# Kernel tuning notes

Hardware: AMD Instinct MI355X
Metric: run time of the kernel (lower is better)

## Reference

```python
import jax, jax.numpy as jnp
import numpy as np
from itertools import product

B, D, H, W = 2, 32, 256, 256
N = 150000
C_IN, C_MID, C_OUT = 16, 32, 64
STRIDE, PAD, K = 2, 1, 3
DO = (D + 2 * PAD - K) // STRIDE + 1
HO = (H + 2 * PAD - K) // STRIDE + 1
WO = (W + 2 * PAD - K) // STRIDE + 1
EPS = 1e-5


def setup_inputs() -> dict:
    key = jax.random.key(0)
    ks = jax.random.split(key, 8)
    # unique active voxel coords via permutation of linear grid indices
    lin = jax.random.permutation(ks[0], B * D * H * W)[:N]
    b = lin // (D * H * W); r = lin % (D * H * W)
    z = r // (H * W); r = r % (H * W)
    y = r // W; x = r % W
    coords = jnp.stack([b, z, y, x], axis=1).astype(jnp.int32)  # [N,4] = (batch,z,y,x)
    feats = jax.random.normal(ks[1], (N, C_IN), jnp.float32)
    W1 = jax.random.normal(ks[2], (27, C_IN, C_MID), jnp.float32) * 0.08
    W2 = jax.random.normal(ks[3], (27, C_MID, C_MID), jnp.float32) * 0.06
    W3 = jax.random.normal(ks[4], (27, C_MID, C_OUT), jnp.float32) * 0.06
    b1 = jnp.zeros((C_MID,), jnp.float32); g1 = jnp.ones((C_MID,), jnp.float32); be1 = jnp.zeros((C_MID,), jnp.float32)
    b2 = jnp.zeros((C_MID,), jnp.float32); g2 = jnp.ones((C_MID,), jnp.float32); be2 = jnp.zeros((C_MID,), jnp.float32)
    b3 = jnp.zeros((C_OUT,), jnp.float32); g3 = jnp.ones((C_OUT,), jnp.float32); be3 = jnp.zeros((C_OUT,), jnp.float32)
    return dict(feats=feats, coords=coords, W1=W1, b1=b1, g1=g1, be1=be1,
                W2=W2, b2=b2, g2=g2, be2=be2, W3=W3, b3=b3, g3=g3, be3=be3)


def _bn_relu(x, g, b):
    # BatchNorm1d (training batch stats, biased var) over active voxels + ReLU
    m = x.mean(0)
    v = ((x - m) ** 2).mean(0)
    return jax.nn.relu((x - m) * jax.lax.rsqrt(v + EPS) * g + b)


def _subm_conv(feats, coords, grid, Wk, bias):
    # submanifold conv: gather neighbor features per kernel offset, GEMM, accumulate
    bb, zz, yy, xx = coords[:, 0], coords[:, 1], coords[:, 2], coords[:, 3]
    acc = jnp.zeros((feats.shape[0], Wk.shape[-1]), feats.dtype)
    for ki, (dz, dy, dx) in enumerate(product((-1, 0, 1), repeat=3)):
        nz, ny, nx = zz + dz, yy + dy, xx + dx
        valid = (nz >= 0) & (nz < D) & (ny >= 0) & (ny < H) & (nx >= 0) & (nx < W)
        lin = ((bb * D + jnp.clip(nz, 0, D - 1)) * H + jnp.clip(ny, 0, H - 1)) * W + jnp.clip(nx, 0, W - 1)
        nidx = jnp.where(valid, grid[lin], -1)
        gathered = jnp.where((nidx >= 0)[:, None], feats[jnp.maximum(nidx, 0)], 0.0)
        acc = acc + gathered @ Wk[ki]
    return acc + bias


def _sparse_down_conv(feats, coords, Wk, bias):
    # stride-2 SparseConv3d as GEMM + scatter-add into downsampled dense grid; mask = active outputs
    bb, zz, yy, xx = coords[:, 0], coords[:, 1], coords[:, 2], coords[:, 3]
    M = B * DO * HO * WO
    out = jnp.zeros((M, Wk.shape[-1]), feats.dtype)
    cnt = jnp.zeros((M,), jnp.int32)
    for ki, (kz, ky, kx) in enumerate(product(range(K), repeat=3)):
        oz, oy, ox = zz + PAD - kz, yy + PAD - ky, xx + PAD - kx
        valid = ((oz % STRIDE == 0) & (oy % STRIDE == 0) & (ox % STRIDE == 0) &
                 (oz >= 0) & (oy >= 0) & (ox >= 0) &
                 (oz // STRIDE < DO) & (oy // STRIDE < HO) & (ox // STRIDE < WO))
        lin = ((bb * DO + jnp.clip(oz // STRIDE, 0, DO - 1)) * HO
               + jnp.clip(oy // STRIDE, 0, HO - 1)) * WO + jnp.clip(ox // STRIDE, 0, WO - 1)
        lin = jnp.where(valid, lin, 0)
        contrib = jnp.where(valid[:, None], feats @ Wk[ki], 0.0)
        out = out.at[lin].add(contrib)
        cnt = cnt.at[lin].add(valid.astype(jnp.int32))
    mask = cnt > 0
    out = jnp.where(mask[:, None], out + bias, 0.0)
    return out, mask


def reference(feats, coords, W1, b1, g1, be1, W2, b2, g2, be2, W3, b3, g3, be3):
    lin0 = ((coords[:, 0] * D + coords[:, 1]) * H + coords[:, 2]) * W + coords[:, 3]
    grid = jnp.full((B * D * H * W,), -1, jnp.int32).at[lin0].set(jnp.arange(N, dtype=jnp.int32))
    x = _bn_relu(_subm_conv(feats, coords, grid, W1, b1), g1, be1)
    x = _bn_relu(_subm_conv(x, coords, grid, W2, b2), g2, be2)
    out, mask = _sparse_down_conv(x, coords, W3, b3)
    nact = jnp.maximum(mask.sum(), 1).astype(out.dtype)
    m = out.sum(0) / nact  # inactive rows are zero
    v = jnp.where(mask[:, None], (out - m) ** 2, 0.0).sum(0) / nact
    out = jax.nn.relu((out - m) * jax.lax.rsqrt(v + EPS) * g3 + be3)
    out = jnp.where(mask[:, None], out, 0.0)
    return out.reshape(B, DO, HO, WO, C_OUT)
```

## Files before the change

kernel.cpp:

```cpp
#include <hip/hip_runtime.h>

#define B_   2
#define D_   32
#define H_   256
#define W_   256
#define N_   150000
#define CIN  16
#define CMID 32
#define COUT 64
#define DO_  16
#define HO_  128
#define WO_  128
#define M_   (B_*DO_*HO_*WO_)
#define EPSf 1e-5f
#define NB_DOWN 8192
#define NREP 64

typedef _Float16 h2 __attribute__((ext_vector_type(2)));
__device__ inline h2 as_h2(unsigned u) { union { unsigned u; h2 h; } x; x.u = u; return x.h; }

#if defined(__has_builtin) && __has_builtin(__builtin_amdgcn_fdot2)
__device__ inline float dot2(unsigned f, unsigned w, float acc) {
    return __builtin_amdgcn_fdot2(as_h2(f), as_h2(w), acc, false);
}
#else
__device__ inline float dot2(unsigned f, unsigned w, float acc) {
    const h2 a = as_h2(f), b = as_h2(w);
    return fmaf((float)a.x, (float)b.x, fmaf((float)a.y, (float)b.y, acc));
}
#endif

__device__ inline unsigned hpk(float a, float b) {
    union { _Float16 h[2]; unsigned u; } x;
    x.h[0] = (_Float16)a; x.h[1] = (_Float16)b; return x.u;
}

__global__ __launch_bounds__(256) void k_scatter(const int* __restrict__ coords,
                                                 int* __restrict__ grid) {
    int i = blockIdx.x * 256 + threadIdx.x;
    if (i >= N_) return;
    const int4 c = *(const int4*)(coords + 4 * (size_t)i);
    grid[((c.x * D_ + c.y) * H_ + c.z) * W_ + c.w] = i;
}

__global__ __launch_bounds__(256) void k_twisth(const float* __restrict__ W1,
                                                const float* __restrict__ W2,
                                                const float* __restrict__ W3,
                                                uint4* __restrict__ Wh1,
                                                uint4* __restrict__ Wh2,
                                                uint4* __restrict__ Wh3) {
    const int t = blockIdx.x * 256 + threadIdx.x;
    if (t < 1728) {
        const int ki = t / 64, r = t % 64, half = r >> 5, sub = r & 31;
        const float* base = W1 + ki * 512 + (half * 8) * 32 + sub;
        uint4 o;
        o.x = hpk(base[0],   base[32]);
        o.y = hpk(base[64],  base[96]);
        o.z = hpk(base[128], base[160]);
        o.w = hpk(base[192], base[224]);
        Wh1[(ki * 2 + half) * 32 + sub] = o;
    } else if (t < 1728 + 3456) {
        const int u = t - 1728;
        const int ki = u / 128, r = u % 128, qh = r >> 5, sub = r & 31;
        const int half = qh >> 1, q = qh & 1;
        const float* base = W2 + ki * 1024 + (half * 16 + q * 8) * 32 + sub;
        uint4 o;
        o.x = hpk(base[0],   base[32]);
        o.y = hpk(base[64],  base[96]);
        o.z = hpk(base[128], base[160]);
        o.w = hpk(base[192], base[224]);
        Wh2[((ki * 2 + half) * 2 + q) * 32 + sub] = o;
    } else if (t < 1728 + 3456 + 6912) {
        const int u = t - 5184;
        const int ki = u / 256, r = u % 256, q = r >> 6, lane = r & 63;
        const float* base = W3 + ki * 2048 + (q * 8) * 64 + lane;
        uint4 o;
        o.x = hpk(base[0],   base[64]);
        o.y = hpk(base[128], base[192]);
        o.z = hpk(base[256], base[320]);
        o.w = hpk(base[384], base[448]);
        Wh3[(ki * 4 + q) * 64 + lane] = o;
    }
}

__global__ __launch_bounds__(256) void k_feat16(const float* __restrict__ F,
                                                unsigned* __restrict__ F16) {
    const int i = blockIdx.x * 256 + threadIdx.x;
    if (i >= N_ * CIN / 4) return;
    const float4 v = ((const float4*)F)[i];
    uint2 o; o.x = hpk(v.x, v.y); o.y = hpk(v.z, v.w);
    ((uint2*)F16)[i] = o;
}

template <int CI>
__global__ __launch_bounds__(256) void k_subm(const unsigned* __restrict__ X16,
                                              const int* __restrict__ coords,
                                              const int* __restrict__ grid,
                                              const uint4* __restrict__ Wh,
                                              const float* __restrict__ bias,
                                              float* __restrict__ Y) {
    constexpr int NQ = CI / 16;
    const int pid  = (blockIdx.x * 256 + threadIdx.x) >> 6;
    const int lane = threadIdx.x & 63;
    const int sub  = lane & 31;
    const int half = lane >> 5;
    const int iA   = pid * 2;

    const int4 cA = *(const int4*)(coords + 4 * (size_t)iA);
    const int4 cB = *(const int4*)(coords + 4 * (size_t)(iA + 1));
    const int4 cc = half ? cB : cA;

    int nidx = -1;
    if (sub < 27) {
        const int nz = cc.y + sub / 9 - 1;
        const int ny = cc.z + (sub / 3) % 3 - 1;
        const int nx = cc.w + sub % 3 - 1;
        if ((unsigned)nz < (unsigned)D_ && (unsigned)ny < (unsigned)H_ &&
            (unsigned)nx < (unsigned)W_)
            nidx = grid[((cc.x * D_ + nz) * H_ + ny) * W_ + nx];
    }
    const unsigned long long act = __ballot(nidx >= 0);
    unsigned int actA = (unsigned int)(act & 0x7FFFFFFull);
    unsigned int actB = (unsigned int)((act >> 32) & 0x7FFFFFFull);

    float accA = 0.f, accB = 0.f;

    while (actA | actB) {
        if (actA) {
            const int ki = __builtin_ctz(actA); actA &= actA - 1;
            const int ni = __shfl(nidx, ki, 64);
            const uint4* __restrict__ f =
                (const uint4*)(X16 + (size_t)ni * (CI / 2) + half * (CI / 4));
            const uint4* __restrict__ wb = Wh + ((size_t)(ki * 2 + half)) * NQ * 32 + sub;
#pragma unroll
            for (int q = 0; q < NQ; ++q) {
                const uint4 fu = f[q];
                const uint4 wu = wb[q * 32];
                accA = dot2(fu.x, wu.x, accA);
                accA = dot2(fu.y, wu.y, accA);
                accA = dot2(fu.z, wu.z, accA);
                accA = dot2(fu.w, wu.w, accA);
            }
        }
        if (actB) {
            const int ki = __builtin_ctz(actB); actB &= actB - 1;
            const int ni = __shfl(nidx, ki + 32, 64);
            const uint4* __restrict__ f =
                (const uint4*)(X16 + (size_t)ni * (CI / 2) + half * (CI / 4));
            const uint4* __restrict__ wb = Wh + ((size_t)(ki * 2 + half)) * NQ * 32 + sub;
#pragma unroll
            for (int q = 0; q < NQ; ++q) {
                const uint4 fu = f[q];
                const uint4 wu = wb[q * 32];
                accB = dot2(fu.x, wu.x, accB);
                accB = dot2(fu.y, wu.y, accB);
                accB = dot2(fu.z, wu.z, accB);
                accB = dot2(fu.w, wu.w, accB);
            }
        }
    }

    accA += __shfl_xor(accA, 32, 64);
    accB += __shfl_xor(accB, 32, 64);
    const float outv = (half ? accB : accA) + bias[sub];
    Y[(size_t)(iA + half) * 32 + sub] = outv;
}

__global__ __launch_bounds__(256) void k_down(const unsigned* __restrict__ X16,
                                              const int* __restrict__ grid,
                                              const uint4* __restrict__ Wh3,
                                              const float* __restrict__ bias,
                                              _Float16* __restrict__ Yh,
                                              unsigned char* __restrict__ mask,
                                              float* __restrict__ slab0,
                                              int* __restrict__ nacts) {
    const int b    = blockIdx.x;
    const int swz  = (b & 7) * (NB_DOWN / 8) + (b >> 3);
    const int tid  = threadIdx.x;
    const int wv   = tid >> 6;
    const int lane = tid & 63;
    const int sub  = lane & 31;
    const int half = lane >> 5;

    const int vox0 = swz * 64;
    const int ox0  = vox0 & 127;
    int t = vox0 >> 7;
    const int oy = t & 127; t >>= 7;
    const int oz = t & 15;
    const int bb = t >> 4;

    __shared__ int   gl[9][132];
    __shared__ float sd[256];
    __shared__ int   scnt[4];

    const int gx0 = 2 * ox0 - 1;
    for (int e = tid; e < 9 * 132; e += 256) {
        const int r  = e / 132, xo = e % 132;
        const int z  = 2 * oz - 1 + r / 3;
        const int y  = 2 * oy - 1 + r % 3;
        const int x  = gx0 + xo;
        int v = -1;
        if ((unsigned)z < (unsigned)D_ && (unsigned)y < (unsigned)H_ &&
            (unsigned)x < (unsigned)W_ && xo < 129)
            v = grid[((bb * D_ + z) * H_ + y) * W_ + x];
        gl[r][xo] = v;
    }
    __syncthreads();

    const int dz = sub / 9, dy = (sub / 3) % 3, dx = sub % 3;
    const int row = (sub < 27) ? dz * 3 + dy : 0;

    const float bv = bias[lane];
    float s = 0.f, s2 = 0.f;
    int cnt = 0;

    for (int it = 0; it < 8; ++it) {
        const int pr = wv * 8 + it;
        const int xo = 2 * (pr * 2 + half) + dx;
        const int nidx = (sub < 27) ? gl[row][xo] : -1;

        const unsigned long long act = __ballot(nidx >= 0);
        unsigned int actA = (unsigned int)(act & 0x7FFFFFFull);
        unsigned int actB = (unsigned int)((act >> 32) & 0x7FFFFFFull);
        const int mkA = actA ? 1 : 0;
        const int mkB = actB ? 1 : 0;

        float accA = 0.f, accB = 0.f;
        while (actA | actB) {
            if (actA) {
                const int ki = __builtin_ctz(actA); actA &= actA - 1;
                const int ni = __builtin_amdgcn_readfirstlane(__shfl(nidx, ki, 64));
                const uint4* __restrict__ fS = (const uint4*)(X16 + (size_t)ni * 16);
                const uint4* __restrict__ wb = Wh3 + (size_t)ki * 256 + lane;
#pragma unroll
                for (int q = 0; q < 4; ++q) {
                    const uint4 fu = fS[q];
                    const uint4 wu = wb[q * 64];
                    accA = dot2(fu.x, wu.x, accA);
                    accA = dot2(fu.y, wu.y, accA);
                    accA = dot2(fu.z, wu.z, accA);
                    accA = dot2(fu.w, wu.w, accA);
                }
            }
            if (actB) {
                const int ki = __builtin_ctz(actB); actB &= actB - 1;
                const int ni = __builtin_amdgcn_readfirstlane(__shfl(nidx, ki + 32, 64));
                const uint4* __restrict__ fS = (const uint4*)(X16 + (size_t)ni * 16);
                const uint4* __restrict__ wb = Wh3 + (size_t)ki * 256 + lane;
#pragma unroll
                for (int q = 0; q < 4; ++q) {
                    const uint4 fu = fS[q];
                    const uint4 wu = wb[q * 64];
                    accB = dot2(fu.x, wu.x, accB);
                    accB = dot2(fu.y, wu.y, accB);
                    accB = dot2(fu.z, wu.z, accB);
                    accB = dot2(fu.w, wu.w, accB);
                }
            }
        }

        const int vA = vox0 + pr * 2;
        const float oA = mkA ? accA + bv : 0.f;
        const float oB = mkB ? accB + bv : 0.f;
        Yh[(size_t)vA * COUT + lane]       = (_Float16)oA;
        Yh[(size_t)(vA + 1) * COUT + lane] = (_Float16)oB;
        if (lane == 0) {
            mask[vA]     = (unsigned char)mkA;
            mask[vA + 1] = (unsigned char)mkB;
            cnt += mkA + mkB;
        }
        s  += oA + oB;
        s2 += oA * oA + oB * oB;
    }

    float* __restrict__ slab = slab0 + (size_t)(b & (NREP - 1)) * 128;
    sd[tid] = s;
    if (lane == 0) scnt[wv] = cnt;
    __syncthreads();
    if (tid < 64) atomicAdd(slab + tid, sd[tid] + sd[tid + 64] + sd[tid + 128] + sd[tid + 192]);
    __syncthreads();
    sd[tid] = s2;
    __syncthreads();
    if (tid < 64) atomicAdd(slab + 64 + tid, sd[tid] + sd[tid + 64] + sd[tid + 128] + sd[tid + 192]);
    if (tid == 0) atomicAdd(nacts + (b & (NREP - 1)), scnt[0] + scnt[1] + scnt[2] + scnt[3]);
}

template <int C>
__global__ __launch_bounds__(256) void k_stats(const float* __restrict__ Y,
                                               long n_elems,
                                               float* __restrict__ slab0) {
    __shared__ float sdata[256];
    const int t = threadIdx.x;
    const long stride = (long)gridDim.x * 256;
    float s = 0.f, s2 = 0.f;
    for (long idx = (long)blockIdx.x * 256 + t; idx < n_elems; idx += stride) {
        const float v = Y[idx];
        s += v; s2 += v * v;
    }
    float* __restrict__ slab = slab0 + (size_t)(blockIdx.x & (NREP - 1)) * 2 * C;
    sdata[t] = s; __syncthreads();
    for (int off = 128; off >= C; off >>= 1) {
        if (t < off) sdata[t] += sdata[t + off];
        __syncthreads();
    }
    if (t < C) atomicAdd(slab + t, sdata[t]);
    __syncthreads();
    sdata[t] = s2; __syncthreads();
    for (int off = 128; off >= C; off >>= 1) {
        if (t < off) sdata[t] += sdata[t + off];
        __syncthreads();
    }
    if (t < C) atomicAdd(slab + C + t, sdata[t]);
}

template <int C>
__global__ void k_finslab(const float* __restrict__ slab0,
                          const float* __restrict__ g,
                          const float* __restrict__ be,
                          float n, float* __restrict__ ss) {
    const int c = threadIdx.x;
    if (c >= C) return;
    float sm = 0.f, s2 = 0.f;
    for (int r = 0; r < NREP; ++r) {
        sm += slab0[r * 2 * C + c];
        s2 += slab0[r * 2 * C + C + c];
    }
    const float m  = sm / n;
    const float v  = s2 / n - m * m;
    const float sc = g[c] * rsqrtf(v + EPSf);
    ss[c]     = sc;
    ss[C + c] = be[c] - m * sc;
}

__global__ void k_finstats3(const float* __restrict__ slab0,
                            const int* __restrict__ nacts,
                            const float* __restrict__ g,
                            const float* __restrict__ be,
                            float* __restrict__ ss) {
    const int c = threadIdx.x;
    if (c >= 64) return;
    float sm = 0.f, s2 = 0.f;
    int na = 0;
    for (int r = 0; r < NREP; ++r) {
        sm += slab0[r * 128 + c];
        s2 += slab0[r * 128 + 64 + c];
        na += nacts[r];
    }
    const float n  = (float)(na > 0 ? na : 1);
    const float m  = sm / n;
    const float v  = s2 / n - m * m;
    const float sc = g[c] * rsqrtf(v + EPSf);
    ss[c]      = sc;
    ss[64 + c] = be[c] - m * sc;
}

template <int C>
__global__ __launch_bounds__(256) void k_norm16(const float* __restrict__ Y,
                                                const float* __restrict__ ss,
                                                unsigned* __restrict__ Xo16, long n4) {
    const long t = (long)blockIdx.x * 256 + threadIdx.x;
    if (t >= n4) return;
    const float4 y = ((const float4*)Y)[t];
    const int ch = (int)((t * 4) % C);
    float ox = fmaxf(fmaf(y.x, ss[ch],     ss[C + ch]),     0.f);
    float oy = fmaxf(fmaf(y.y, ss[ch + 1], ss[C + ch + 1]), 0.f);
    float oz = fmaxf(fmaf(y.z, ss[ch + 2], ss[C + ch + 2]), 0.f);
    float ow = fmaxf(fmaf(y.w, ss[ch + 3], ss[C + ch + 3]), 0.f);
    uint2 o; o.x = hpk(ox, oy); o.y = hpk(oz, ow);
    ((uint2*)Xo16)[t] = o;
}

__global__ __launch_bounds__(256) void k_norm3(const _Float16* __restrict__ Yh,
                                               const unsigned char* __restrict__ mask,
                                               const float* __restrict__ ss,
                                               float* __restrict__ out) {
    const long n4 = (long)M_ * COUT / 4;
    const long t = (long)blockIdx.x * 256 + threadIdx.x;
    if (t >= n4) return;
    const long vox = t >> 4;
    const int ch = (int)((t * 4) & 63);
    float4 o;
    if (mask[vox]) {
        const uint2 yu = *(const uint2*)(Yh + t * 4);
        const h2 ylo = as_h2(yu.x), yhi = as_h2(yu.y);
        o.x = fmaxf(fmaf((float)ylo.x, ss[ch],     ss[64 + ch]),     0.f);
        o.y = fmaxf(fmaf((float)ylo.y, ss[ch + 1], ss[64 + ch + 1]), 0.f);
        o.z = fmaxf(fmaf((float)yhi.x, ss[ch + 2], ss[64 + ch + 2]), 0.f);
        o.w = fmaxf(fmaf((float)yhi.y, ss[ch + 3], ss[64 + ch + 3]), 0.f);
    } else {
        o.x = o.y = o.z = o.w = 0.f;
    }
    ((float4*)out)[t] = o;
}

extern "C" void kernel_launch(void* const* d_in, const int* in_sizes, int n_in,
                              void* d_out, int out_size, void* d_ws, size_t ws_size,
                              hipStream_t stream) {
    const float* feats = (const float*)d_in[0];
    const int*   coords = (const int*)d_in[1];
    const float* W1 = (const float*)d_in[2];
    const float* b1 = (const float*)d_in[3];
    const float* g1 = (const float*)d_in[4];
    const float* be1 = (const float*)d_in[5];
    const float* W2 = (const float*)d_in[6];
    const float* b2 = (const float*)d_in[7];
    const float* g2 = (const float*)d_in[8];
    const float* be2 = (const float*)d_in[9];
    const float* W3 = (const float*)d_in[10];
    const float* b3 = (const float*)d_in[11];
    const float* g3 = (const float*)d_in[12];
    const float* be3 = (const float*)d_in[13];
    float* out = (float*)d_out;

    char* ws = (char*)d_ws;
    const size_t gridBytes = (size_t)B_ * D_ * H_ * W_ * 4;
    const size_t bufBytes  = (size_t)N_ * CMID * 4;
    const size_t bufHBytes = (size_t)N_ * CMID * 2;
    const size_t YhBytes   = (size_t)M_ * COUT * 2;
    int*       grid   = (int*)ws;
    float*     bufA   = (float*)(ws + gridBytes);
    unsigned*  bufH   = (unsigned*)(ws + gridBytes + bufBytes);
    unsigned*  feat16 = (unsigned*)(ws + gridBytes + bufBytes + bufHBytes);
    _Float16*  Yh     = (_Float16*)(ws + gridBytes + bufBytes + bufHBytes +
                                    (size_t)N_ * CIN * 2);
    unsigned char* mask = (unsigned char*)(ws + gridBytes + bufBytes + bufHBytes +
                                           (size_t)N_ * CIN * 2 + YhBytes);
    float* stats = (float*)(ws + gridBytes + bufBytes + bufHBytes +
                            (size_t)N_ * CIN * 2 + YhBytes + (size_t)M_);

    float* ss1   = stats;
    float* ss2   = stats + 64;
    float* ss3   = stats + 128;
    float* slab1 = stats + 1024;
    float* slab2 = stats + 1024 + NREP * 64;
    float* slab3 = stats + 1024 + NREP * 128;
    int*   nacts = (int*)(stats + 1024 + NREP * 256);
    uint4* Wh1 = (uint4*)(stats + 32768);
    uint4* Wh2 = Wh1 + 1728;
    uint4* Wh3 = Wh2 + 3456;

    hipMemsetAsync(grid, 0xFF, gridBytes, stream);
    hipMemsetAsync(stats + 1024, 0, (NREP * 256 + NREP) * 4, stream);

    k_scatter<<<(N_ + 255) / 256, 256, 0, stream>>>(coords, grid);
    k_twisth<<<(12096 + 255) / 256, 256, 0, stream>>>(W1, W2, W3, Wh1, Wh2, Wh3);
    k_feat16<<<(N_ * CIN / 4 + 255) / 256, 256, 0, stream>>>(feats, feat16);

    const int nb_subm = 75000 / 4;
    k_subm<CIN><<<nb_subm, 256, 0, stream>>>(feat16, coords, grid, Wh1, b1, bufA);
    k_stats<CMID><<<512, 256, 0, stream>>>(bufA, (long)N_ * CMID, slab1);
    k_finslab<CMID><<<1, 64, 0, stream>>>(slab1, g1, be1, (float)N_, ss1);
    k_norm16<CMID><<<(N_ * CMID / 4 + 255) / 256, 256, 0, stream>>>(bufA, ss1, bufH,
                                                                    (long)N_ * CMID / 4);

    k_subm<CMID><<<nb_subm, 256, 0, stream>>>(bufH, coords, grid, Wh2, b2, bufA);
    k_stats<CMID><<<512, 256, 0, stream>>>(bufA, (long)N_ * CMID, slab2);
    k_finslab<CMID><<<1, 64, 0, stream>>>(slab2, g2, be2, (float)N_, ss2);
    k_norm16<CMID><<<(N_ * CMID / 4 + 255) / 256, 256, 0, stream>>>(bufA, ss2, bufH,
                                                                    (long)N_ * CMID / 4);

    k_down<<<NB_DOWN, 256, 0, stream>>>(bufH, grid, Wh3, b3, Yh, mask, slab3, nacts);
    k_finstats3<<<1, 64, 0, stream>>>(slab3, nacts, g3, be3, ss3);
    k_norm3<<<(M_ * COUT / 4) / 256, 256, 0, stream>>>(Yh, mask, ss3, out);
}
```

Baseline: 265.0 us.

## Fuse BN stats into submanifold conv, store fp16 pre-norm, process four voxels per wave

Each subm conv block now reduces per-channel sum and sum-of-squares in shared memory and atomically adds them into the stats slab, which removes the separate k_stats pass over the fp32 output. The intermediate output is stored as fp16 instead of fp32, halving the write and re-read traffic for k_norm16. Both subm and down-conv kernels now handle four voxels per wave instead of two, interleaving more independent gather chains to hide latency. In exchange there is fp16 rounding before the batch-norm stats and apply, plus more atomics and block syncs.

```diff
diff --git a/kernel.cpp b/kernel.cpp
--- a/kernel.cpp
+++ b/kernel.cpp
@@ -98,72 +98,103 @@
                                               const int* __restrict__ grid,
                                               const uint4* __restrict__ Wh,
                                               const float* __restrict__ bias,
-                                              float* __restrict__ Y) {
+                                              _Float16* __restrict__ Yp,
+                                              float* __restrict__ slab0) {
     constexpr int NQ = CI / 16;
-    const int pid  = (blockIdx.x * 256 + threadIdx.x) >> 6;
+    const int wid  = (blockIdx.x * 256 + threadIdx.x) >> 6;
     const int lane = threadIdx.x & 63;
     const int sub  = lane & 31;
     const int half = lane >> 5;
-    const int iA   = pid * 2;
-
-    const int4 cA = *(const int4*)(coords + 4 * (size_t)iA);
-    const int4 cB = *(const int4*)(coords + 4 * (size_t)(iA + 1));
-    const int4 cc = half ? cB : cA;
-
-    int nidx = -1;
-    if (sub < 27) {
-        const int nz = cc.y + sub / 9 - 1;
-        const int ny = cc.z + (sub / 3) % 3 - 1;
-        const int nx = cc.w + sub % 3 - 1;
-        if ((unsigned)nz < (unsigned)D_ && (unsigned)ny < (unsigned)H_ &&
-            (unsigned)nx < (unsigned)W_)
-            nidx = grid[((cc.x * D_ + nz) * H_ + ny) * W_ + nx];
-    }
-    const unsigned long long act = __ballot(nidx >= 0);
-    unsigned int actA = (unsigned int)(act & 0x7FFFFFFull);
-    unsigned int actB = (unsigned int)((act >> 32) & 0x7FFFFFFull);
-
-    float accA = 0.f, accB = 0.f;
-
-    while (actA | actB) {
-        if (actA) {
-            const int ki = __builtin_ctz(actA); actA &= actA - 1;
-            const int ni = __shfl(nidx, ki, 64);
-            const uint4* __restrict__ f =
-                (const uint4*)(X16 + (size_t)ni * (CI / 2) + half * (CI / 4));
-            const uint4* __restrict__ wb = Wh + ((size_t)(ki * 2 + half)) * NQ * 32 + sub;
+    const int i0   = wid * 4;
+
+    int nidx01 = -1, nidx23 = -1;
+    {
+        const int4 cc = *(const int4*)(coords + 4 * (size_t)(i0 + half));
+        if (sub < 27) {
+            const int nz = cc.y + sub / 9 - 1;
+            const int ny = cc.z + (sub / 3) % 3 - 1;
+            const int nx = cc.w + sub % 3 - 1;
+            if ((unsigned)nz < (unsigned)D_ && (unsigned)ny < (unsigned)H_ &&
+                (unsigned)nx < (unsigned)W_)
+                nidx01 = grid[((cc.x * D_ + nz) * H_ + ny) * W_ + nx];
+        }
+    }
+    {
+        const int4 cc = *(const int4*)(coords + 4 * (size_t)(i0 + 2 + half));
+        if (sub < 27) {
+            const int nz = cc.y + sub / 9 - 1;
+            const int ny = cc.z + (sub / 3) % 3 - 1;
+            const int nx = cc.w + sub % 3 - 1;
+            if ((unsigned)nz < (unsigned)D_ && (unsigned)ny < (unsigned)H_ &&
+                (unsigned)nx < (unsigned)W_)
+                nidx23 = grid[((cc.x * D_ + nz) * H_ + ny) * W_ + nx];
+        }
+    }
+    const unsigned long long a01 = __ballot(nidx01 >= 0);
+    const unsigned long long a23 = __ballot(nidx23 >= 0);
+    unsigned m0 = (unsigned)a01 & 0x7FFFFFFu;
+    unsigned m1 = (unsigned)(a01 >> 32) & 0x7FFFFFFu;
+    unsigned m2 = (unsigned)a23 & 0x7FFFFFFu;
+    unsigned m3 = (unsigned)(a23 >> 32) & 0x7FFFFFFu;
+
+    float acc0 = 0.f, acc1 = 0.f, acc2 = 0.f, acc3 = 0.f;
+
+    auto tap = [&](int ki, int ni, float& acc) {
+        const uint4* __restrict__ f =
+            (const uint4*)(X16 + (size_t)ni * (CI / 2) + half * (CI / 4));
+        const uint4* __restrict__ wb = Wh + ((size_t)(ki * 2 + half)) * NQ * 32 + sub;
 #pragma unroll
-            for (int q = 0; q < NQ; ++q) {
-                const uint4 fu = f[q];
-                const uint4 wu = wb[q * 32];
-                accA = dot2(fu.x, wu.x, accA);
-                accA = dot2(fu.y, wu.y, accA);
-                accA = dot2(fu.z, wu.z, accA);
-                accA = dot2(fu.w, wu.w, accA);
-            }
-        }
-        if (actB) {
-            const int ki = __builtin_ctz(actB); actB &= actB - 1;
-            const int ni = __shfl(nidx, ki + 32, 64);
-            const uint4* __restrict__ f =
-                (const uint4*)(X16 + (size_t)ni * (CI / 2) + half * (CI / 4));
-            const uint4* __restrict__ wb = Wh + ((size_t)(ki * 2 + half)) * NQ * 32 + sub;
+        for (int q = 0; q < NQ; ++q) {
+            const uint4 fu = f[q];
+            const uint4 wu = wb[q * 32];
+            acc = dot2(fu.x, wu.x, acc);
+            acc = dot2(fu.y, wu.y, acc);
+            acc = dot2(fu.z, wu.z, acc);
+            acc = dot2(fu.w, wu.w, acc);
+        }
+    };
+
+    while (m0 | m1 | m2 | m3) {
+        if (m0) { const int ki = __builtin_ctz(m0); m0 &= m0 - 1;
+                  tap(ki, __shfl(nidx01, ki, 64),      acc0); }
+        if (m1) { const int ki = __builtin_ctz(m1); m1 &= m1 - 1;
+                  tap(ki, __shfl(nidx01, ki + 32, 64), acc1); }
+        if (m2) { const int ki = __builtin_ctz(m2); m2 &= m2 - 1;
+                  tap(ki, __shfl(nidx23, ki, 64),      acc2); }
+        if (m3) { const int ki = __builtin_ctz(m3); m3 &= m3 - 1;
+                  tap(ki, __shfl(nidx23, ki + 32, 64), acc3); }
+    }
+
+    acc0 += __shfl_xor(acc0, 32, 64);
+    acc1 += __shfl_xor(acc1, 32, 64);
+    acc2 += __shfl_xor(acc2, 32, 64);
+    acc3 += __shfl_xor(acc3, 32, 64);
+    const float bv  = bias[sub];
+    const float o01 = (half ? acc1 : acc0) + bv;
+    const float o23 = (half ? acc3 : acc2) + bv;
+    Yp[(size_t)(i0 + half) * 32 + sub]     = (_Float16)o01;
+    Yp[(size_t)(i0 + 2 + half) * 32 + sub] = (_Float16)o23;
+
+    __shared__ float sd[256];
+    const int tid = threadIdx.x;
+    float* __restrict__ slab = slab0 + (size_t)(blockIdx.x & (NREP - 1)) * 64;
+    sd[tid] = o01 + o23;
+    __syncthreads();
+    if (tid < 32) {
+        float t = 0.f;
 #pragma unroll
-            for (int q = 0; q < NQ; ++q) {
-                const uint4 fu = f[q];
-                const uint4 wu = wb[q * 32];
-                accB = dot2(fu.x, wu.x, accB);
-                accB = dot2(fu.y, wu.y, accB);
-                accB = dot2(fu.z, wu.z, accB);
-                accB = dot2(fu.w, wu.w, accB);
-            }
-        }
-    }
-
-    accA += __shfl_xor(accA, 32, 64);
-    accB += __shfl_xor(accB, 32, 64);
-    const float outv = (half ? accB : accA) + bias[sub];
-    Y[(size_t)(iA + half) * 32 + sub] = outv;
+        for (int k = 0; k < 8; ++k) t += sd[tid + 32 * k];
+        atomicAdd(slab + tid, t);
+    }
+    __syncthreads();
+    sd[tid] = o01 * o01 + o23 * o23;
+    __syncthreads();
+    if (tid < 32) {
+        float t = 0.f;
+#pragma unroll
+        for (int k = 0; k < 8; ++k) t += sd[tid + 32 * k];
+        atomicAdd(slab + 32 + tid, t);
+    }
 }
 
 __global__ __launch_bounds__(256) void k_down(const unsigned* __restrict__ X16,
@@ -214,63 +245,63 @@
     float s = 0.f, s2 = 0.f;
     int cnt = 0;
 
-    for (int it = 0; it < 8; ++it) {
-        const int pr = wv * 8 + it;
-        const int xo = 2 * (pr * 2 + half) + dx;
-        const int nidx = (sub < 27) ? gl[row][xo] : -1;
-
-        const unsigned long long act = __ballot(nidx >= 0);
-        unsigned int actA = (unsigned int)(act & 0x7FFFFFFull);
-        unsigned int actB = (unsigned int)((act >> 32) & 0x7FFFFFFull);
-        const int mkA = actA ? 1 : 0;
-        const int mkB = actB ? 1 : 0;
-
-        float accA = 0.f, accB = 0.f;
-        while (actA | actB) {
-            if (actA) {
-                const int ki = __builtin_ctz(actA); actA &= actA - 1;
-                const int ni = __builtin_amdgcn_readfirstlane(__shfl(nidx, ki, 64));
-                const uint4* __restrict__ fS = (const uint4*)(X16 + (size_t)ni * 16);
-                const uint4* __restrict__ wb = Wh3 + (size_t)ki * 256 + lane;
+    auto tap = [&](int ki, int ni, float& acc) {
+        const uint4* __restrict__ fS = (const uint4*)(X16 + (size_t)ni * 16);
+        const uint4* __restrict__ wb = Wh3 + (size_t)ki * 256 + lane;
 #pragma unroll
-                for (int q = 0; q < 4; ++q) {
-                    const uint4 fu = fS[q];
-                    const uint4 wu = wb[q * 64];
-                    accA = dot2(fu.x, wu.x, accA);
-                    accA = dot2(fu.y, wu.y, accA);
-                    accA = dot2(fu.z, wu.z, accA);
-                    accA = dot2(fu.w, wu.w, accA);
-                }
-            }
-            if (actB) {
-                const int ki = __builtin_ctz(actB); actB &= actB - 1;
-                const int ni = __builtin_amdgcn_readfirstlane(__shfl(nidx, ki + 32, 64));
-                const uint4* __restrict__ fS = (const uint4*)(X16 + (size_t)ni * 16);
-                const uint4* __restrict__ wb = Wh3 + (size_t)ki * 256 + lane;
-#pragma unroll
-                for (int q = 0; q < 4; ++q) {
-                    const uint4 fu = fS[q];
-                    const uint4 wu = wb[q * 64];
-                    accB = dot2(fu.x, wu.x, accB);
-                    accB = dot2(fu.y, wu.y, accB);
-                    accB = dot2(fu.z, wu.z, accB);
-                    accB = dot2(fu.w, wu.w, accB);
-                }
-            }
-        }
-
-        const int vA = vox0 + pr * 2;
-        const float oA = mkA ? accA + bv : 0.f;
-        const float oB = mkB ? accB + bv : 0.f;
-        Yh[(size_t)vA * COUT + lane]       = (_Float16)oA;
-        Yh[(size_t)(vA + 1) * COUT + lane] = (_Float16)oB;
+        for (int q = 0; q < 4; ++q) {
+            const uint4 fu = fS[q];
+            const uint4 wu = wb[q * 64];
+            acc = dot2(fu.x, wu.x, acc);
+            acc = dot2(fu.y, wu.y, acc);
+            acc = dot2(fu.z, wu.z, acc);
+            acc = dot2(fu.w, wu.w, acc);
+        }
+    };
+
+    for (int it = 0; it < 4; ++it) {
+        const int v0 = wv * 16 + it * 4;
+        const int n01 = (sub < 27) ? gl[row][2 * (v0 + half) + dx] : -1;
+        const int n23 = (sub < 27) ? gl[row][2 * (v0 + 2 + half) + dx] : -1;
+        const unsigned long long a01 = __ballot(n01 >= 0);
+        const unsigned long long a23 = __ballot(n23 >= 0);
+        unsigned m0 = (unsigned)a01 & 0x7FFFFFFu;
+        unsigned m1 = (unsigned)(a01 >> 32) & 0x7FFFFFFu;
+        unsigned m2 = (unsigned)a23 & 0x7FFFFFFu;
+        unsigned m3 = (unsigned)(a23 >> 32) & 0x7FFFFFFu;
+        const int mk0 = m0 ? 1 : 0, mk1 = m1 ? 1 : 0;
+        const int mk2 = m2 ? 1 : 0, mk3 = m3 ? 1 : 0;
+
+        float ac0 = 0.f, ac1 = 0.f, ac2 = 0.f, ac3 = 0.f;
+        while (m0 | m1 | m2 | m3) {
+            if (m0) { const int ki = __builtin_ctz(m0); m0 &= m0 - 1;
+                      tap(ki, __builtin_amdgcn_readfirstlane(__shfl(n01, ki, 64)),      ac0); }
+            if (m1) { const int ki = __builtin_ctz(m1); m1 &= m1 - 1;
+                      tap(ki, __builtin_amdgcn_readfirstlane(__shfl(n01, ki + 32, 64)), ac1); }
+            if (m2) { const int ki = __builtin_ctz(m2); m2 &= m2 - 1;
+                      tap(ki, __builtin_amdgcn_readfirstlane(__shfl(n23, ki, 64)),      ac2); }
+            if (m3) { const int ki = __builtin_ctz(m3); m3 &= m3 - 1;
+                      tap(ki, __builtin_amdgcn_readfirstlane(__shfl(n23, ki + 32, 64)), ac3); }
+        }
+
+        const int vg = vox0 + v0;
+        const float o0 = mk0 ? ac0 + bv : 0.f;
+        const float o1 = mk1 ? ac1 + bv : 0.f;
+        const float o2 = mk2 ? ac2 + bv : 0.f;
+        const float o3 = mk3 ? ac3 + bv : 0.f;
+        Yh[(size_t)vg * COUT + lane]       = (_Float16)o0;
+        Yh[(size_t)(vg + 1) * COUT + lane] = (_Float16)o1;
+        Yh[(size_t)(vg + 2) * COUT + lane] = (_Float16)o2;
+        Yh[(size_t)(vg + 3) * COUT + lane] = (_Float16)o3;
         if (lane == 0) {
-            mask[vA]     = (unsigned char)mkA;
-            mask[vA + 1] = (unsigned char)mkB;
-            cnt += mkA + mkB;
-        }
-        s  += oA + oB;
-        s2 += oA * oA + oB * oB;
+            mask[vg]     = (unsigned char)mk0;
+            mask[vg + 1] = (unsigned char)mk1;
+            mask[vg + 2] = (unsigned char)mk2;
+            mask[vg + 3] = (unsigned char)mk3;
+            cnt += mk0 + mk1 + mk2 + mk3;
+        }
+        s  += o0 + o1 + o2 + o3;
+        s2 += o0 * o0 + o1 * o1 + o2 * o2 + o3 * o3;
     }
 
     float* __restrict__ slab = slab0 + (size_t)(b & (NREP - 1)) * 128;
@@ -283,34 +314,6 @@
     __syncthreads();
     if (tid < 64) atomicAdd(slab + 64 + tid, sd[tid] + sd[tid + 64] + sd[tid + 128] + sd[tid + 192]);
     if (tid == 0) atomicAdd(nacts + (b & (NREP - 1)), scnt[0] + scnt[1] + scnt[2] + scnt[3]);
-}
-
-template <int C>
-__global__ __launch_bounds__(256) void k_stats(const float* __restrict__ Y,
-                                               long n_elems,
-                                               float* __restrict__ slab0) {
-    __shared__ float sdata[256];
-    const int t = threadIdx.x;
-    const long stride = (long)gridDim.x * 256;
-    float s = 0.f, s2 = 0.f;
-    for (long idx = (long)blockIdx.x * 256 + t; idx < n_elems; idx += stride) {
-        const float v = Y[idx];
-        s += v; s2 += v * v;
-    }
-    float* __restrict__ slab = slab0 + (size_t)(blockIdx.x & (NREP - 1)) * 2 * C;
-    sdata[t] = s; __syncthreads();
-    for (int off = 128; off >= C; off >>= 1) {
-        if (t < off) sdata[t] += sdata[t + off];
-        __syncthreads();
-    }
-    if (t < C) atomicAdd(slab + t, sdata[t]);
-    __syncthreads();
-    sdata[t] = s2; __syncthreads();
-    for (int off = 128; off >= C; off >>= 1) {
-        if (t < off) sdata[t] += sdata[t + off];
-        __syncthreads();
-    }
-    if (t < C) atomicAdd(slab + C + t, sdata[t]);
 }
 
 template <int C>
@@ -355,17 +358,18 @@
 }
 
 template <int C>
-__global__ __launch_bounds__(256) void k_norm16(const float* __restrict__ Y,
+__global__ __launch_bounds__(256) void k_norm16(const unsigned* __restrict__ Yp2,
                                                 const float* __restrict__ ss,
                                                 unsigned* __restrict__ Xo16, long n4) {
     const long t = (long)blockIdx.x * 256 + threadIdx.x;
     if (t >= n4) return;
-    const float4 y = ((const float4*)Y)[t];
+    const uint2 y = ((const uint2*)Yp2)[t];
+    const h2 lo = as_h2(y.x), hi = as_h2(y.y);
     const int ch = (int)((t * 4) % C);
-    float ox = fmaxf(fmaf(y.x, ss[ch],     ss[C + ch]),     0.f);
-    float oy = fmaxf(fmaf(y.y, ss[ch + 1], ss[C + ch + 1]), 0.f);
-    float oz = fmaxf(fmaf(y.z, ss[ch + 2], ss[C + ch + 2]), 0.f);
-    float ow = fmaxf(fmaf(y.w, ss[ch + 3], ss[C + ch + 3]), 0.f);
+    float ox = fmaxf(fmaf((float)lo.x, ss[ch],     ss[C + ch]),     0.f);
+    float oy = fmaxf(fmaf((float)lo.y, ss[ch + 1], ss[C + ch + 1]), 0.f);
+    float oz = fmaxf(fmaf((float)hi.x, ss[ch + 2], ss[C + ch + 2]), 0.f);
+    float ow = fmaxf(fmaf((float)hi.y, ss[ch + 3], ss[C + ch + 3]), 0.f);
     uint2 o; o.x = hpk(ox, oy); o.y = hpk(oz, ow);
     ((uint2*)Xo16)[t] = o;
 }
@@ -414,19 +418,16 @@
 
     char* ws = (char*)d_ws;
     const size_t gridBytes = (size_t)B_ * D_ * H_ * W_ * 4;
-    const size_t bufBytes  = (size_t)N_ * CMID * 4;
-    const size_t bufHBytes = (size_t)N_ * CMID * 2;
+    const size_t f16Bytes  = (size_t)N_ * CIN * 2;
+    const size_t bufPBytes = (size_t)N_ * CMID * 2;
     const size_t YhBytes   = (size_t)M_ * COUT * 2;
     int*       grid   = (int*)ws;
-    float*     bufA   = (float*)(ws + gridBytes);
-    unsigned*  bufH   = (unsigned*)(ws + gridBytes + bufBytes);
-    unsigned*  feat16 = (unsigned*)(ws + gridBytes + bufBytes + bufHBytes);
-    _Float16*  Yh     = (_Float16*)(ws + gridBytes + bufBytes + bufHBytes +
-                                    (size_t)N_ * CIN * 2);
-    unsigned char* mask = (unsigned char*)(ws + gridBytes + bufBytes + bufHBytes +
-                                           (size_t)N_ * CIN * 2 + YhBytes);
-    float* stats = (float*)(ws + gridBytes + bufBytes + bufHBytes +
-                            (size_t)N_ * CIN * 2 + YhBytes + (size_t)M_);
+    unsigned*  feat16 = (unsigned*)(ws + gridBytes);
+    _Float16*  bufP   = (_Float16*)(ws + gridBytes + f16Bytes);
+    unsigned*  bufH   = (unsigned*)(ws + gridBytes + f16Bytes + bufPBytes);
+    _Float16*  Yh     = (_Float16*)(ws + gridBytes + f16Bytes + 2 * bufPBytes);
+    unsigned char* mask = (unsigned char*)(ws + gridBytes + f16Bytes + 2 * bufPBytes + YhBytes);
+    float* stats = (float*)(ws + gridBytes + f16Bytes + 2 * bufPBytes + YhBytes + (size_t)M_);
 
     float* ss1   = stats;
     float* ss2   = stats + 64;
@@ -446,18 +447,16 @@
     k_twisth<<<(12096 + 255) / 256, 256, 0, stream>>>(W1, W2, W3, Wh1, Wh2, Wh3);
     k_feat16<<<(N_ * CIN / 4 + 255) / 256, 256, 0, stream>>>(feats, feat16);
 
-    const int nb_subm = 75000 / 4;
-    k_subm<CIN><<<nb_subm, 256, 0, stream>>>(feat16, coords, grid, Wh1, b1, bufA);
-    k_stats<CMID><<<512, 256, 0, stream>>>(bufA, (long)N_ * CMID, slab1);
+    const int nb_subm = N_ / 16;
+    k_subm<CIN><<<nb_subm, 256, 0, stream>>>(feat16, coords, grid, Wh1, b1, bufP, slab1);
     k_finslab<CMID><<<1, 64, 0, stream>>>(slab1, g1, be1, (float)N_, ss1);
-    k_norm16<CMID><<<(N_ * CMID / 4 + 255) / 256, 256, 0, stream>>>(bufA, ss1, bufH,
-                                                                    (long)N_ * CMID / 4);
-
-    k_subm<CMID><<<nb_subm, 256, 0, stream>>>(bufH, coords, grid, Wh2, b2, bufA);
-    k_stats<CMID><<<512, 256, 0, stream>>>(bufA, (long)N_ * CMID, slab2);
+    k_norm16<CMID><<<(N_ * CMID / 4 + 255) / 256, 256, 0, stream>>>(
+        (const unsigned*)bufP, ss1, bufH, (long)N_ * CMID / 4);
+
+    k_subm<CMID><<<nb_subm, 256, 0, stream>>>(bufH, coords, grid, Wh2, b2, bufP, slab2);
     k_finslab<CMID><<<1, 64, 0, stream>>>(slab2, g2, be2, (float)N_, ss2);
-    k_norm16<CMID><<<(N_ * CMID / 4 + 255) / 256, 256, 0, stream>>>(bufA, ss2, bufH,
-                                                                    (long)N_ * CMID / 4);
+    k_norm16<CMID><<<(N_ * CMID / 4 + 255) / 256, 256, 0, stream>>>(
+        (const unsigned*)bufP, ss2, bufH, (long)N_ * CMID / 4);
 
     k_down<<<NB_DOWN, 256, 0, stream>>>(bufH, grid, Wh3, b3, Yh, mask, slab3, nacts);
     k_finstats3<<<1, 64, 0, stream>>>(slab3, nacts, g3, be3, ss3);
```

New measurement: 239.7 us. 9.5% less time.
